# Optimization experiments

Hardware: AMD Instinct MI355X
Metric: run time of the kernel (lower is better)

Reference implementation:

```python
import jax, jax.numpy as jnp
import numpy as np

UFEAT_DIM = 256
MAPFEAT_DIM = 64


def setup_inputs() -> dict:
    key = jax.random.key(0)
    k1, k2, k3, k4 = jax.random.split(key, 4)
    ufeat = jax.random.normal(k1, (32, 512, UFEAT_DIM), dtype=jnp.float32)
    mapfeat = jax.random.normal(k2, (32, 4096, MAPFEAT_DIM), dtype=jnp.float32)
    # weight_norm(Linear, dim=None): W = g * V / ||V||_F, g scalar
    v_w = jax.random.normal(k3, (MAPFEAT_DIM, UFEAT_DIM), dtype=jnp.float32) * 0.05
    g = jnp.asarray(1.0, dtype=jnp.float32)
    b = jax.random.normal(k4, (MAPFEAT_DIM,), dtype=jnp.float32) * 0.05
    return {"ufeat": ufeat, "mapfeat": mapfeat, "v_w": v_w, "g": g, "b": b}


def reference(ufeat, mapfeat, v_w, g, b):
    # weight-normalized linear (dim=None -> scalar g over Frobenius norm)
    w = g * v_w / jnp.linalg.norm(v_w)
    proj = jax.nn.relu(jnp.einsum("bud,md->bum", ufeat, w) + b)  # [B, U, M]
    norm = jnp.sqrt(jnp.asarray(MAPFEAT_DIM, dtype=proj.dtype))
    # broadcast dot-product over spatial map, expressed as a batched matmul
    logit = jnp.einsum("bum,bsm->bus", proj, mapfeat) / norm  # [B, U, x*y]
    return logit
```

## Files before the change

### kernel.cpp

```cpp
#include <hip/hip_runtime.h>
#include <hip/hip_bf16.h>

typedef __bf16 bf16x8 __attribute__((ext_vector_type(8)));
typedef float  f32x16 __attribute__((ext_vector_type(16)));
typedef float  f32x4  __attribute__((ext_vector_type(4)));

#define UF_D 256
#define MAP_M 64
#define B_DIM 32
#define U_DIM 512
#define S_DIM 4096

__global__ __launch_bounds__(256) void prep_conv_kernel(
    const float* __restrict__ v_w, const float* __restrict__ g,
    const float* __restrict__ b, const float* __restrict__ mapfeat,
    __bf16* __restrict__ w_bf16, float* __restrict__ b_s,
    __bf16* __restrict__ map_bf16)
{
    const int t = threadIdx.x;
    if (blockIdx.x == 0) {
        __shared__ float red[256];
        const f32x4* v4 = (const f32x4*)v_w;
        float ss = 0.f;
        for (int i = t; i < 4096; i += 256) {
            f32x4 v = v4[i];
            ss += v.x * v.x + v.y * v.y + v.z * v.z + v.w * v.w;
        }
        red[t] = ss;
        __syncthreads();
        for (int s = 128; s > 0; s >>= 1) {
            if (t < s) red[t] += red[t + s];
            __syncthreads();
        }
        const float scale = g[0] / (sqrtf(red[0]) * 8.0f);
        for (int i = t; i < 4096; i += 256) {
            f32x4 v = v4[i];
            w_bf16[4 * i + 0] = (__bf16)(v.x * scale);
            w_bf16[4 * i + 1] = (__bf16)(v.y * scale);
            w_bf16[4 * i + 2] = (__bf16)(v.z * scale);
            w_bf16[4 * i + 3] = (__bf16)(v.w * scale);
        }
        if (t < MAP_M) b_s[t] = b[t] * 0.125f;
    } else {
        const int NC = (B_DIM * S_DIM * MAP_M) / 8;
        const f32x4* m4 = (const f32x4*)mapfeat;
        bf16x8* o8 = (bf16x8*)map_bf16;
        for (int c = (blockIdx.x - 1) * 256 + t; c < NC; c += 255 * 256) {
            f32x4 q0 = __builtin_nontemporal_load(&m4[2 * c]);
            f32x4 q1 = __builtin_nontemporal_load(&m4[2 * c + 1]);
            bf16x8 o;
            o[0] = (__bf16)q0.x; o[1] = (__bf16)q0.y;
            o[2] = (__bf16)q0.z; o[3] = (__bf16)q0.w;
            o[4] = (__bf16)q1.x; o[5] = (__bf16)q1.y;
            o[6] = (__bf16)q1.z; o[7] = (__bf16)q1.w;
            o8[c] = o;
        }
    }
}

__global__ __launch_bounds__(256) void proj_kernel(
    const float* __restrict__ ufeat,
    const __bf16* __restrict__ w,
    const float* __restrict__ b_s,
    __bf16* __restrict__ proj)
{
    const int wave = threadIdx.x >> 6;
    const int lane = threadIdx.x & 63;
    const int r  = lane & 31;
    const int kh = lane >> 5;
    const int wr = wave >> 1, wc = wave & 1;
    const int row0 = blockIdx.x * 64 + wr * 32;
    const int col0 = wc * 32;

    f32x16 acc = {};
    const float*  ap = ufeat + (size_t)(row0 + r) * UF_D + kh * 8;
    const __bf16* wp = w + (col0 + r) * UF_D + kh * 8;

#pragma unroll
    for (int k = 0; k < UF_D; k += 16) {
        f32x4 a01 = __builtin_nontemporal_load((const f32x4*)(ap + k));
        f32x4 a23 = __builtin_nontemporal_load((const f32x4*)(ap + k + 4));
        bf16x8 af;
        af[0] = (__bf16)a01.x; af[1] = (__bf16)a01.y;
        af[2] = (__bf16)a01.z; af[3] = (__bf16)a01.w;
        af[4] = (__bf16)a23.x; af[5] = (__bf16)a23.y;
        af[6] = (__bf16)a23.z; af[7] = (__bf16)a23.w;
        bf16x8 wf = *(const bf16x8*)(wp + k);
        acc = __builtin_amdgcn_mfma_f32_32x32x16_bf16(af, wf, acc, 0, 0, 0);
    }

#pragma unroll
    for (int j = 0; j < 16; ++j) {
        const int rl = (j & 3) + 8 * (j >> 2) + 4 * kh;
        const size_t row = row0 + rl;
        const int col = col0 + r;
        float v = acc[j] + b_s[col];
        proj[row * MAP_M + col] = (__bf16)fmaxf(v, 0.f);
    }
}

__global__ __launch_bounds__(256) void logit_kernel(
    const __bf16* __restrict__ proj,
    const __bf16* __restrict__ map,
    float* __restrict__ out)
{
    const int vid = (blockIdx.x & 7) * 512 + (blockIdx.x >> 3);
    const int ut = vid & 3;
    const int st = (vid >> 2) & 31;
    const int b  = vid >> 7;

    const int wave = threadIdx.x >> 6;
    const int lane = threadIdx.x & 63;
    const int wr = wave >> 1, wc = wave & 1;
    const int r  = lane & 31;
    const int kh = lane >> 5;

    const int u0 = ut * 128 + wr * 64;
    const int s0 = st * 128 + wc * 64;

    const __bf16* A  = proj + (size_t)b * U_DIM * MAP_M;
    const __bf16* Bm = map  + (size_t)b * S_DIM * MAP_M;

    f32x16 acc00 = {}, acc01 = {}, acc10 = {}, acc11 = {};

    const __bf16* a0p = A  + (size_t)(u0 + r)      * MAP_M + kh * 8;
    const __bf16* a1p = A  + (size_t)(u0 + 32 + r) * MAP_M + kh * 8;
    const __bf16* b0p = Bm + (size_t)(s0 + r)      * MAP_M + kh * 8;
    const __bf16* b1p = Bm + (size_t)(s0 + 32 + r) * MAP_M + kh * 8;

#pragma unroll
    for (int k = 0; k < MAP_M; k += 16) {
        bf16x8 a0 = *(const bf16x8*)(a0p + k);
        bf16x8 a1 = *(const bf16x8*)(a1p + k);
        bf16x8 f0 = *(const bf16x8*)(b0p + k);
        bf16x8 f1 = *(const bf16x8*)(b1p + k);
        acc00 = __builtin_amdgcn_mfma_f32_32x32x16_bf16(a0, f0, acc00, 0, 0, 0);
        acc01 = __builtin_amdgcn_mfma_f32_32x32x16_bf16(a0, f1, acc01, 0, 0, 0);
        acc10 = __builtin_amdgcn_mfma_f32_32x32x16_bf16(a1, f0, acc10, 0, 0, 0);
        acc11 = __builtin_amdgcn_mfma_f32_32x32x16_bf16(a1, f1, acc11, 0, 0, 0);
    }

    float* O = out + (size_t)b * U_DIM * S_DIM;
#pragma unroll
    for (int j = 0; j < 16; ++j) {
        const int rl = (j & 3) + 8 * (j >> 2) + 4 * kh;
        const size_t row0 = u0 + rl;
        const size_t row1 = u0 + 32 + rl;
        __builtin_nontemporal_store(acc00[j], &O[row0 * S_DIM + s0 + r]);
        __builtin_nontemporal_store(acc01[j], &O[row0 * S_DIM + s0 + 32 + r]);
        __builtin_nontemporal_store(acc10[j], &O[row1 * S_DIM + s0 + r]);
        __builtin_nontemporal_store(acc11[j], &O[row1 * S_DIM + s0 + 32 + r]);
    }
}

extern "C" void kernel_launch(void* const* d_in, const int* in_sizes, int n_in,
                              void* d_out, int out_size, void* d_ws, size_t ws_size,
                              hipStream_t stream) {
    const float* ufeat   = (const float*)d_in[0];
    const float* mapfeat = (const float*)d_in[1];
    const float* v_w     = (const float*)d_in[2];
    const float* g       = (const float*)d_in[3];
    const float* b       = (const float*)d_in[4];
    float* out = (float*)d_out;

    __bf16* w_bf16   = (__bf16*)d_ws;
    float*  b_s      = (float*)((char*)d_ws + 32768);
    __bf16* proj     = (__bf16*)((char*)d_ws + 65536);
    __bf16* map_bf16 = (__bf16*)((char*)d_ws + 65536 + 2097152);

    prep_conv_kernel<<<256, 256, 0, stream>>>(v_w, g, b, mapfeat, w_bf16, b_s, map_bf16);
    proj_kernel<<<256, 256, 0, stream>>>(ufeat, w_bf16, b_s, proj);
    logit_kernel<<<B_DIM * 32 * 4, 256, 0, stream>>>(proj, map_bf16, out);
}
```

Baseline: 328.5 us.

## Fuse weight-norm prep into projection and convert mapfeat to bf16 in logit kernel

Removes the separate prep kernel. Each projection block now recomputes the Frobenius norm of v_w and scales the weights on the fly, using 16x16x32 MFMA tiles across 1024 blocks. The logit kernel reads fp32 mapfeat directly and converts it to bf16 in registers, so the 32 MB read plus 16 MB write for the bf16 copy of mapfeat goes away. In exchange, each logit tile re-reads fp32 map data across the 4 u-tiles (2x bytes per load), and every projection block repeats the norm reduction.

```diff
diff --git a/kernel.cpp b/kernel.cpp
--- a/kernel.cpp
+++ b/kernel.cpp
@@ -11,15 +11,17 @@
 #define U_DIM 512
 #define S_DIM 4096
 
-__global__ __launch_bounds__(256) void prep_conv_kernel(
-    const float* __restrict__ v_w, const float* __restrict__ g,
-    const float* __restrict__ b, const float* __restrict__ mapfeat,
-    __bf16* __restrict__ w_bf16, float* __restrict__ b_s,
-    __bf16* __restrict__ map_bf16)
+__global__ __launch_bounds__(256) void proj_kernel(
+    const float* __restrict__ ufeat,
+    const float* __restrict__ v_w,
+    const float* __restrict__ g,
+    const float* __restrict__ b,
+    __bf16* __restrict__ proj)
 {
     const int t = threadIdx.x;
-    if (blockIdx.x == 0) {
-        __shared__ float red[256];
+
+    __shared__ float red[256];
+    {
         const f32x4* v4 = (const f32x4*)v_w;
         float ss = 0.f;
         for (int i = t; i < 4096; i += 256) {
@@ -32,76 +34,50 @@
             if (t < s) red[t] += red[t + s];
             __syncthreads();
         }
-        const float scale = g[0] / (sqrtf(red[0]) * 8.0f);
-        for (int i = t; i < 4096; i += 256) {
-            f32x4 v = v4[i];
-            w_bf16[4 * i + 0] = (__bf16)(v.x * scale);
-            w_bf16[4 * i + 1] = (__bf16)(v.y * scale);
-            w_bf16[4 * i + 2] = (__bf16)(v.z * scale);
-            w_bf16[4 * i + 3] = (__bf16)(v.w * scale);
-        }
-        if (t < MAP_M) b_s[t] = b[t] * 0.125f;
-    } else {
-        const int NC = (B_DIM * S_DIM * MAP_M) / 8;
-        const f32x4* m4 = (const f32x4*)mapfeat;
-        bf16x8* o8 = (bf16x8*)map_bf16;
-        for (int c = (blockIdx.x - 1) * 256 + t; c < NC; c += 255 * 256) {
-            f32x4 q0 = __builtin_nontemporal_load(&m4[2 * c]);
-            f32x4 q1 = __builtin_nontemporal_load(&m4[2 * c + 1]);
-            bf16x8 o;
-            o[0] = (__bf16)q0.x; o[1] = (__bf16)q0.y;
-            o[2] = (__bf16)q0.z; o[3] = (__bf16)q0.w;
-            o[4] = (__bf16)q1.x; o[5] = (__bf16)q1.y;
-            o[6] = (__bf16)q1.z; o[7] = (__bf16)q1.w;
-            o8[c] = o;
-        }
     }
-}
+    const float scale = g[0] / (sqrtf(red[0]) * 8.0f);
 
-__global__ __launch_bounds__(256) void proj_kernel(
-    const float* __restrict__ ufeat,
-    const __bf16* __restrict__ w,
-    const float* __restrict__ b_s,
-    __bf16* __restrict__ proj)
-{
-    const int wave = threadIdx.x >> 6;
-    const int lane = threadIdx.x & 63;
-    const int r  = lane & 31;
-    const int kh = lane >> 5;
-    const int wr = wave >> 1, wc = wave & 1;
-    const int row0 = blockIdx.x * 64 + wr * 32;
-    const int col0 = wc * 32;
+    const int wave = t >> 6;
+    const int lane = t & 63;
+    const int r  = lane & 15;
+    const int kq = lane >> 4;
+    const int row0 = blockIdx.x * 16;
+    const int col0 = wave * 16;
 
-    f32x16 acc = {};
-    const float*  ap = ufeat + (size_t)(row0 + r) * UF_D + kh * 8;
-    const __bf16* wp = w + (col0 + r) * UF_D + kh * 8;
+    f32x4 acc = {};
+    const float* ap = ufeat + (size_t)(row0 + r) * UF_D + kq * 8;
+    const float* wp = v_w   + (size_t)(col0 + r) * UF_D + kq * 8;
 
 #pragma unroll
-    for (int k = 0; k < UF_D; k += 16) {
-        f32x4 a01 = __builtin_nontemporal_load((const f32x4*)(ap + k));
-        f32x4 a23 = __builtin_nontemporal_load((const f32x4*)(ap + k + 4));
-        bf16x8 af;
-        af[0] = (__bf16)a01.x; af[1] = (__bf16)a01.y;
-        af[2] = (__bf16)a01.z; af[3] = (__bf16)a01.w;
-        af[4] = (__bf16)a23.x; af[5] = (__bf16)a23.y;
-        af[6] = (__bf16)a23.z; af[7] = (__bf16)a23.w;
-        bf16x8 wf = *(const bf16x8*)(wp + k);
-        acc = __builtin_amdgcn_mfma_f32_32x32x16_bf16(af, wf, acc, 0, 0, 0);
+    for (int k = 0; k < UF_D; k += 32) {
+        f32x4 a0 = *(const f32x4*)(ap + k);
+        f32x4 a1 = *(const f32x4*)(ap + k + 4);
+        f32x4 w0 = *(const f32x4*)(wp + k);
+        f32x4 w1 = *(const f32x4*)(wp + k + 4);
+        bf16x8 af, wf;
+        af[0] = (__bf16)a0.x; af[1] = (__bf16)a0.y;
+        af[2] = (__bf16)a0.z; af[3] = (__bf16)a0.w;
+        af[4] = (__bf16)a1.x; af[5] = (__bf16)a1.y;
+        af[6] = (__bf16)a1.z; af[7] = (__bf16)a1.w;
+        wf[0] = (__bf16)(w0.x * scale); wf[1] = (__bf16)(w0.y * scale);
+        wf[2] = (__bf16)(w0.z * scale); wf[3] = (__bf16)(w0.w * scale);
+        wf[4] = (__bf16)(w1.x * scale); wf[5] = (__bf16)(w1.y * scale);
+        wf[6] = (__bf16)(w1.z * scale); wf[7] = (__bf16)(w1.w * scale);
+        acc = __builtin_amdgcn_mfma_f32_16x16x32_bf16(af, wf, acc, 0, 0, 0);
     }
 
 #pragma unroll
-    for (int j = 0; j < 16; ++j) {
-        const int rl = (j & 3) + 8 * (j >> 2) + 4 * kh;
-        const size_t row = row0 + rl;
+    for (int j = 0; j < 4; ++j) {
+        const int row = row0 + kq * 4 + j;
         const int col = col0 + r;
-        float v = acc[j] + b_s[col];
-        proj[row * MAP_M + col] = (__bf16)fmaxf(v, 0.f);
+        float v = acc[j] + b[col] * 0.125f;
+        proj[(size_t)row * MAP_M + col] = (__bf16)fmaxf(v, 0.f);
     }
 }
 
 __global__ __launch_bounds__(256) void logit_kernel(
     const __bf16* __restrict__ proj,
-    const __bf16* __restrict__ map,
+    const float* __restrict__ map,
     float* __restrict__ out)
 {
     const int vid = (blockIdx.x & 7) * 512 + (blockIdx.x >> 3);
@@ -119,21 +95,32 @@
     const int s0 = st * 128 + wc * 64;
 
     const __bf16* A  = proj + (size_t)b * U_DIM * MAP_M;
-    const __bf16* Bm = map  + (size_t)b * S_DIM * MAP_M;
+    const float*  Bm = map  + (size_t)b * S_DIM * MAP_M;
 
     f32x16 acc00 = {}, acc01 = {}, acc10 = {}, acc11 = {};
 
     const __bf16* a0p = A  + (size_t)(u0 + r)      * MAP_M + kh * 8;
     const __bf16* a1p = A  + (size_t)(u0 + 32 + r) * MAP_M + kh * 8;
-    const __bf16* b0p = Bm + (size_t)(s0 + r)      * MAP_M + kh * 8;
-    const __bf16* b1p = Bm + (size_t)(s0 + 32 + r) * MAP_M + kh * 8;
+    const float*  b0p = Bm + (size_t)(s0 + r)      * MAP_M + kh * 8;
+    const float*  b1p = Bm + (size_t)(s0 + 32 + r) * MAP_M + kh * 8;
 
 #pragma unroll
     for (int k = 0; k < MAP_M; k += 16) {
         bf16x8 a0 = *(const bf16x8*)(a0p + k);
         bf16x8 a1 = *(const bf16x8*)(a1p + k);
-        bf16x8 f0 = *(const bf16x8*)(b0p + k);
-        bf16x8 f1 = *(const bf16x8*)(b1p + k);
+        f32x4 q0 = *(const f32x4*)(b0p + k);
+        f32x4 q1 = *(const f32x4*)(b0p + k + 4);
+        f32x4 q2 = *(const f32x4*)(b1p + k);
+        f32x4 q3 = *(const f32x4*)(b1p + k + 4);
+        bf16x8 f0, f1;
+        f0[0] = (__bf16)q0.x; f0[1] = (__bf16)q0.y;
+        f0[2] = (__bf16)q0.z; f0[3] = (__bf16)q0.w;
+        f0[4] = (__bf16)q1.x; f0[5] = (__bf16)q1.y;
+        f0[6] = (__bf16)q1.z; f0[7] = (__bf16)q1.w;
+        f1[0] = (__bf16)q2.x; f1[1] = (__bf16)q2.y;
+        f1[2] = (__bf16)q2.z; f1[3] = (__bf16)q2.w;
+        f1[4] = (__bf16)q3.x; f1[5] = (__bf16)q3.y;
+        f1[6] = (__bf16)q3.z; f1[7] = (__bf16)q3.w;
         acc00 = __builtin_amdgcn_mfma_f32_32x32x16_bf16(a0, f0, acc00, 0, 0, 0);
         acc01 = __builtin_amdgcn_mfma_f32_32x32x16_bf16(a0, f1, acc01, 0, 0, 0);
         acc10 = __builtin_amdgcn_mfma_f32_32x32x16_bf16(a1, f0, acc10, 0, 0, 0);
@@ -163,12 +150,8 @@
     const float* b       = (const float*)d_in[4];
     float* out = (float*)d_out;
 
-    __bf16* w_bf16   = (__bf16*)d_ws;
-    float*  b_s      = (float*)((char*)d_ws + 32768);
-    __bf16* proj     = (__bf16*)((char*)d_ws + 65536);
-    __bf16* map_bf16 = (__bf16*)((char*)d_ws + 65536 + 2097152);
+    __bf16* proj = (__bf16*)d_ws;
 
-    prep_conv_kernel<<<256, 256, 0, stream>>>(v_w, g, b, mapfeat, w_bf16, b_s, map_bf16);
-    proj_kernel<<<256, 256, 0, stream>>>(ufeat, w_bf16, b_s, proj);
-    logit_kernel<<<B_DIM * 32 * 4, 256, 0, stream>>>(proj, map_bf16, out);
+    proj_kernel<<<1024, 256, 0, stream>>>(ufeat, v_w, g, b, proj);
+    logit_kernel<<<B_DIM * 32 * 4, 256, 0, stream>>>(proj, mapfeat, out);
 }
```

New measurement: 366.5 us. +11.6%, slower.
